# Performance work log

Measured on AMD Instinct MI355X. Metric: run time of the kernel, lower is better.

Reference implementation:

```python
import jax, jax.numpy as jnp
import numpy as np


def setup_inputs() -> dict:
    key = jax.random.key(0)
    k1, k2, k3 = jax.random.split(key, 3)
    N, D_IN, D_OUT = 16384, 512, 128
    inputs = jax.random.normal(k1, (N, D_IN), dtype=jnp.float32)
    adj = jax.random.uniform(k2, (N, N), dtype=jnp.float32)
    # Glorot-uniform init as in weight_variable_glorot
    init_range = np.sqrt(6.0 / (D_IN + D_OUT))
    weights = jax.random.uniform(k3, (D_IN, D_OUT), dtype=jnp.float32,
                                 minval=-init_range, maxval=init_range)
    return {"inputs": inputs, "adj": adj, "weights": weights}


def reference(inputs, adj, weights):
    # x = inputs.to_dense(); x = x @ W; out = adj @ x
    x = jnp.matmul(inputs, weights)      # [N, D_out]
    outputs = jnp.matmul(adj, x)         # [N, D_out]
    return outputs
```

## Files before the change

kernel.cpp:

```cpp
#include <hip/hip_runtime.h>

#define NN 16384
#define DIN 512
#define DOUT 128

typedef __bf16 bf16x8 __attribute__((ext_vector_type(8)));
typedef float floatx4 __attribute__((ext_vector_type(4)));

__device__ __forceinline__ unsigned short f2bf(float f) {
    unsigned u = __builtin_bit_cast(unsigned, f);
    u += 0x7FFFu + ((u >> 16) & 1u);
    return (unsigned short)(u >> 16);
}

__global__ __launch_bounds__(256) void xw_kernel(
        const float* __restrict__ inp, const float* __restrict__ w,
        unsigned short* __restrict__ xT) {
    __shared__ float sIn[32][68];
    __shared__ float sW[64][128];
    const int tid = threadIdx.x;
    const int n0 = blockIdx.x * 32;
    const int tn = tid >> 4;
    const int td = tid & 15;

    float acc[2][8];
#pragma unroll
    for (int i = 0; i < 2; ++i)
#pragma unroll
        for (int j = 0; j < 8; ++j) acc[i][j] = 0.f;

    for (int c0 = 0; c0 < DIN; c0 += 64) {
        __syncthreads();
#pragma unroll
        for (int p = 0; p < 2; ++p) {
            int s = tid + p * 256;
            int row = s >> 4, c4 = (s & 15) << 2;
            *(float4*)&sIn[row][c4] =
                *(const float4*)&inp[(size_t)(n0 + row) * DIN + c0 + c4];
        }
#pragma unroll
        for (int p = 0; p < 8; ++p) {
            int s = tid + p * 256;
            int row = s >> 5, c4 = (s & 31) << 2;
            *(float4*)&sW[row][c4] =
                *(const float4*)&w[(size_t)(c0 + row) * DOUT + c4];
        }
        __syncthreads();
#pragma unroll 8
        for (int cc = 0; cc < 64; ++cc) {
            float a0 = sIn[tn * 2 + 0][cc];
            float a1 = sIn[tn * 2 + 1][cc];
            float4 b0 = *(const float4*)&sW[cc][td * 8];
            float4 b1 = *(const float4*)&sW[cc][td * 8 + 4];
            float bb[8] = {b0.x, b0.y, b0.z, b0.w, b1.x, b1.y, b1.z, b1.w};
#pragma unroll
            for (int j = 0; j < 8; ++j) {
                acc[0][j] += a0 * bb[j];
                acc[1][j] += a1 * bb[j];
            }
        }
    }
#pragma unroll
    for (int i = 0; i < 2; ++i)
#pragma unroll
        for (int j = 0; j < 8; ++j) {
            int d = td * 8 + j;
            xT[(size_t)d * NN + n0 + tn * 2 + i] = f2bf(acc[i][j]);
        }
}

__global__ __launch_bounds__(512, 2) void adj_gemm(
        const float* __restrict__ adj, const unsigned short* __restrict__ xT,
        float* __restrict__ out) {
    __shared__ unsigned short As[64][72];
    __shared__ unsigned short Bs[128][72];
    const int tid  = threadIdx.x;
    const int m0   = blockIdx.x * 64;
    const int w    = tid >> 6;
    const int lane = tid & 63;
    const int rt   = w & 3;
    const int cg   = w >> 2;
    const int lm   = lane & 15;
    const int quad = lane >> 4;

    const int arow = tid >> 4;
    const int ac4  = (tid & 15) << 2;
    const int brow = tid >> 3;
    const int bc8  = (tid & 7) << 3;

    const floatx4 zero = {0.f, 0.f, 0.f, 0.f};
    floatx4 acc[4] = {zero, zero, zero, zero};

    float4 ra[2];
    uint4  rb[2];
#pragma unroll
    for (int p = 0; p < 2; ++p)
        ra[p] = *(const float4*)&adj[(size_t)(m0 + arow + p * 32) * NN + ac4];
#pragma unroll
    for (int p = 0; p < 2; ++p)
        rb[p] = *(const uint4*)&xT[(size_t)(brow + p * 64) * NN + bc8];

    for (int kt = 0; kt < NN / 64; ++kt) {
        __syncthreads();
#pragma unroll
        for (int p = 0; p < 2; ++p) {
            ushort4 h;
            h.x = f2bf(ra[p].x); h.y = f2bf(ra[p].y);
            h.z = f2bf(ra[p].z); h.w = f2bf(ra[p].w);
            *(ushort4*)&As[arow + p * 32][ac4] = h;
        }
#pragma unroll
        for (int p = 0; p < 2; ++p)
            *(uint4*)&Bs[brow + p * 64][bc8] = rb[p];
        __syncthreads();
        if (kt + 1 < NN / 64) {
            const int k0 = (kt + 1) * 64;
#pragma unroll
            for (int p = 0; p < 2; ++p)
                ra[p] = *(const float4*)&adj[(size_t)(m0 + arow + p * 32) * NN + k0 + ac4];
#pragma unroll
            for (int p = 0; p < 2; ++p)
                rb[p] = *(const uint4*)&xT[(size_t)(brow + p * 64) * NN + k0 + bc8];
        }
#pragma unroll
        for (int kk = 0; kk < 2; ++kk) {
            bf16x8 a = *(const bf16x8*)&As[rt * 16 + lm][kk * 32 + quad * 8];
#pragma unroll
            for (int t = 0; t < 4; ++t) {
                bf16x8 b = *(const bf16x8*)&Bs[cg * 64 + t * 16 + lm][kk * 32 + quad * 8];
                acc[t] = __builtin_amdgcn_mfma_f32_16x16x32_bf16(a, b, acc[t], 0, 0, 0);
            }
        }
    }
#pragma unroll
    for (int t = 0; t < 4; ++t)
#pragma unroll
        for (int r = 0; r < 4; ++r)
            out[(size_t)(m0 + rt * 16 + quad * 4 + r) * DOUT + cg * 64 + t * 16 + lm] =
                acc[t][r];
}

extern "C" void kernel_launch(void* const* d_in, const int* in_sizes, int n_in,
                              void* d_out, int out_size, void* d_ws, size_t ws_size,
                              hipStream_t stream) {
    const float* inputs  = (const float*)d_in[0];
    const float* adj     = (const float*)d_in[1];
    const float* weights = (const float*)d_in[2];
    float* out = (float*)d_out;
    unsigned short* xT = (unsigned short*)d_ws;

    xw_kernel<<<NN / 32, 256, 0, stream>>>(inputs, weights, xT);
    adj_gemm<<<NN / 64, 512, 0, stream>>>(adj, xT, out);
}
```

Measured before the change: 1.749 ms.

## Pre-swizzle X into MFMA fragment layout, drop LDS, and split-K the adj GEMM

The xw kernel now writes X in a fragment-ordered bf16 layout, so the adj GEMM can load B operands straight from global into registers without LDS staging or barriers. Each wave handles 16 rows against all 128 output columns, with register double-buffering of adj and X fragments. K is split in two across blockIdx.y into fp32 partial buffers, and a separate reduce kernel sums them. The aim is to remove LDS round-trips and syncs and to raise parallelism. The cost is an extra 16 MB of partial writes and reads, a third launch, and uncoalesced per-row adj loads (32 bytes per lane spread across rows).

```diff
diff --git a/kernel.cpp b/kernel.cpp
--- a/kernel.cpp
+++ b/kernel.cpp
@@ -3,6 +3,9 @@
 #define NN 16384
 #define DIN 512
 #define DOUT 128
+#define SPLITK 2
+#define KHALF (NN / SPLITK)
+#define NK32 (KHALF / 32)
 
 typedef __bf16 bf16x8 __attribute__((ext_vector_type(8)));
 typedef float floatx4 __attribute__((ext_vector_type(4)));
@@ -13,30 +16,36 @@
     return (unsigned short)(u >> 16);
 }
 
+__device__ __forceinline__ unsigned pk2(float lo, float hi) {
+    return (unsigned)f2bf(lo) | ((unsigned)f2bf(hi) << 16);
+}
+
 __global__ __launch_bounds__(256) void xw_kernel(
         const float* __restrict__ inp, const float* __restrict__ w,
-        unsigned short* __restrict__ xT) {
-    __shared__ float sIn[32][68];
+        unsigned short* __restrict__ xTf) {
+    __shared__ float sInT[64][36];
     __shared__ float sW[64][128];
     const int tid = threadIdx.x;
     const int n0 = blockIdx.x * 32;
-    const int tn = tid >> 4;
-    const int td = tid & 15;
+    const int ng = tid >> 6;
+    const int dp = tid & 63;
 
-    float acc[2][8];
+    float acc[8][2];
 #pragma unroll
-    for (int i = 0; i < 2; ++i)
-#pragma unroll
-        for (int j = 0; j < 8; ++j) acc[i][j] = 0.f;
+    for (int i = 0; i < 8; ++i) { acc[i][0] = 0.f; acc[i][1] = 0.f; }
 
     for (int c0 = 0; c0 < DIN; c0 += 64) {
         __syncthreads();
 #pragma unroll
         for (int p = 0; p < 2; ++p) {
             int s = tid + p * 256;
-            int row = s >> 4, c4 = (s & 15) << 2;
-            *(float4*)&sIn[row][c4] =
-                *(const float4*)&inp[(size_t)(n0 + row) * DIN + c0 + c4];
+            int row = s >> 4;
+            int c4 = (s & 15) << 2;
+            float4 v = *(const float4*)&inp[(size_t)(n0 + row) * DIN + c0 + c4];
+            sInT[c4 + 0][row] = v.x;
+            sInT[c4 + 1][row] = v.y;
+            sInT[c4 + 2][row] = v.z;
+            sInT[c4 + 3][row] = v.w;
         }
 #pragma unroll
         for (int p = 0; p < 8; ++p) {
@@ -46,98 +55,103 @@
                 *(const float4*)&w[(size_t)(c0 + row) * DOUT + c4];
         }
         __syncthreads();
-#pragma unroll 8
+#pragma unroll 4
         for (int cc = 0; cc < 64; ++cc) {
-            float a0 = sIn[tn * 2 + 0][cc];
-            float a1 = sIn[tn * 2 + 1][cc];
-            float4 b0 = *(const float4*)&sW[cc][td * 8];
-            float4 b1 = *(const float4*)&sW[cc][td * 8 + 4];
-            float bb[8] = {b0.x, b0.y, b0.z, b0.w, b1.x, b1.y, b1.z, b1.w};
+            float4 a0 = *(const float4*)&sInT[cc][ng * 8];
+            float4 a1 = *(const float4*)&sInT[cc][ng * 8 + 4];
+            float2 b = *(const float2*)&sW[cc][dp * 2];
+            float av[8] = {a0.x, a0.y, a0.z, a0.w, a1.x, a1.y, a1.z, a1.w};
 #pragma unroll
-            for (int j = 0; j < 8; ++j) {
-                acc[0][j] += a0 * bb[j];
-                acc[1][j] += a1 * bb[j];
+            for (int i = 0; i < 8; ++i) {
+                acc[i][0] += av[i] * b.x;
+                acc[i][1] += av[i] * b.y;
             }
         }
     }
 #pragma unroll
-    for (int i = 0; i < 2; ++i)
-#pragma unroll
-        for (int j = 0; j < 8; ++j) {
-            int d = td * 8 + j;
-            xT[(size_t)d * NN + n0 + tn * 2 + i] = f2bf(acc[i][j]);
-        }
+    for (int j = 0; j < 2; ++j) {
+        int d = dp * 2 + j;
+        uint4 u;
+        u.x = pk2(acc[0][j], acc[1][j]);
+        u.y = pk2(acc[2][j], acc[3][j]);
+        u.z = pk2(acc[4][j], acc[5][j]);
+        u.w = pk2(acc[6][j], acc[7][j]);
+        size_t off16 = ((size_t)blockIdx.x * 8 + (d >> 4)) * 64
+                       + (ng * 16 + (d & 15));
+        ((uint4*)xTf)[off16] = u;
+    }
 }
 
-__global__ __launch_bounds__(512, 2) void adj_gemm(
-        const float* __restrict__ adj, const unsigned short* __restrict__ xT,
-        float* __restrict__ out) {
-    __shared__ unsigned short As[64][72];
-    __shared__ unsigned short Bs[128][72];
-    const int tid  = threadIdx.x;
-    const int m0   = blockIdx.x * 64;
-    const int w    = tid >> 6;
+__global__ __launch_bounds__(256, 2) void adj_gemm_f(
+        const float* __restrict__ adj, const unsigned short* __restrict__ xTf,
+        float* __restrict__ part) {
+    const int tid = threadIdx.x;
+    const int w = tid >> 6;
     const int lane = tid & 63;
-    const int rt   = w & 3;
-    const int cg   = w >> 2;
-    const int lm   = lane & 15;
+    const int lm = lane & 15;
     const int quad = lane >> 4;
+    const int m0 = blockIdx.x * 64;
+    const int sk = blockIdx.y;
+    const int row = m0 + w * 16 + lm;
 
-    const int arow = tid >> 4;
-    const int ac4  = (tid & 15) << 2;
-    const int brow = tid >> 3;
-    const int bc8  = (tid & 7) << 3;
+    const float* ap = adj + (size_t)row * NN + (size_t)sk * KHALF + quad * 8;
+    const uint4* bp = (const uint4*)xTf + (size_t)sk * NK32 * 512 + lane;
 
-    const floatx4 zero = {0.f, 0.f, 0.f, 0.f};
-    floatx4 acc[4] = {zero, zero, zero, zero};
+    floatx4 acc[8];
+#pragma unroll
+    for (int t = 0; t < 8; ++t) acc[t] = (floatx4){0.f, 0.f, 0.f, 0.f};
 
-    float4 ra[2];
-    uint4  rb[2];
+    float4 a0A, a1A; uint4 bA[8];
+    float4 a0B, a1B; uint4 bB[8];
+
+#define LOADK(S, kk) do {                                                    \
+        const float* _a = ap + (size_t)(kk) * 32;                            \
+        a0##S = *(const float4*)_a;                                          \
+        a1##S = *(const float4*)(_a + 4);                                    \
+        const uint4* _b = bp + (size_t)(kk) * 512;                           \
+        _Pragma("unroll")                                                    \
+        for (int t = 0; t < 8; ++t) b##S[t] = _b[t * 64];                    \
+    } while (0)
+
+#define COMPUTE(S) do {                                                      \
+        bf16x8 a;                                                            \
+        a[0] = (__bf16)a0##S.x; a[1] = (__bf16)a0##S.y;                      \
+        a[2] = (__bf16)a0##S.z; a[3] = (__bf16)a0##S.w;                      \
+        a[4] = (__bf16)a1##S.x; a[5] = (__bf16)a1##S.y;                      \
+        a[6] = (__bf16)a1##S.z; a[7] = (__bf16)a1##S.w;                      \
+        _Pragma("unroll")                                                    \
+        for (int t = 0; t < 8; ++t)                                          \
+            acc[t] = __builtin_amdgcn_mfma_f32_16x16x32_bf16(                \
+                a, __builtin_bit_cast(bf16x8, b##S[t]), acc[t], 0, 0, 0);    \
+    } while (0)
+
+    LOADK(A, 0);
+    for (int k = 0; k < NK32; k += 2) {
+        LOADK(B, k + 1);
+        COMPUTE(A);
+        if (k + 2 < NK32) LOADK(A, k + 2);
+        COMPUTE(B);
+    }
+#undef LOADK
+#undef COMPUTE
+
+    float* po = part + (size_t)sk * NN * DOUT;
 #pragma unroll
-    for (int p = 0; p < 2; ++p)
-        ra[p] = *(const float4*)&adj[(size_t)(m0 + arow + p * 32) * NN + ac4];
-#pragma unroll
-    for (int p = 0; p < 2; ++p)
-        rb[p] = *(const uint4*)&xT[(size_t)(brow + p * 64) * NN + bc8];
-
-    for (int kt = 0; kt < NN / 64; ++kt) {
-        __syncthreads();
-#pragma unroll
-        for (int p = 0; p < 2; ++p) {
-            ushort4 h;
-            h.x = f2bf(ra[p].x); h.y = f2bf(ra[p].y);
-            h.z = f2bf(ra[p].z); h.w = f2bf(ra[p].w);
-            *(ushort4*)&As[arow + p * 32][ac4] = h;
-        }
-#pragma unroll
-        for (int p = 0; p < 2; ++p)
-            *(uint4*)&Bs[brow + p * 64][bc8] = rb[p];
-        __syncthreads();
-        if (kt + 1 < NN / 64) {
-            const int k0 = (kt + 1) * 64;
-#pragma unroll
-            for (int p = 0; p < 2; ++p)
-                ra[p] = *(const float4*)&adj[(size_t)(m0 + arow + p * 32) * NN + k0 + ac4];
-#pragma unroll
-            for (int p = 0; p < 2; ++p)
-                rb[p] = *(const uint4*)&xT[(size_t)(brow + p * 64) * NN + k0 + bc8];
-        }
-#pragma unroll
-        for (int kk = 0; kk < 2; ++kk) {
-            bf16x8 a = *(const bf16x8*)&As[rt * 16 + lm][kk * 32 + quad * 8];
-#pragma unroll
-            for (int t = 0; t < 4; ++t) {
-                bf16x8 b = *(const bf16x8*)&Bs[cg * 64 + t * 16 + lm][kk * 32 + quad * 8];
-                acc[t] = __builtin_amdgcn_mfma_f32_16x16x32_bf16(a, b, acc[t], 0, 0, 0);
-            }
-        }
-    }
-#pragma unroll
-    for (int t = 0; t < 4; ++t)
+    for (int t = 0; t < 8; ++t)
 #pragma unroll
         for (int r = 0; r < 4; ++r)
-            out[(size_t)(m0 + rt * 16 + quad * 4 + r) * DOUT + cg * 64 + t * 16 + lm] =
+            po[(size_t)(m0 + w * 16 + quad * 4 + r) * DOUT + t * 16 + lm] =
                 acc[t][r];
+}
+
+__global__ __launch_bounds__(256) void reduce_k(
+        const float* __restrict__ part, float* __restrict__ out) {
+    size_t i = (size_t)blockIdx.x * 256 + threadIdx.x;
+    const float4* p0 = (const float4*)part;
+    const float4* p1 = (const float4*)(part + (size_t)NN * DOUT);
+    float4 a = p0[i], b = p1[i];
+    float4 r = {a.x + b.x, a.y + b.y, a.z + b.z, a.w + b.w};
+    ((float4*)out)[i] = r;
 }
 
 extern "C" void kernel_launch(void* const* d_in, const int* in_sizes, int n_in,
@@ -147,8 +161,11 @@
     const float* adj     = (const float*)d_in[1];
     const float* weights = (const float*)d_in[2];
     float* out = (float*)d_out;
-    unsigned short* xT = (unsigned short*)d_ws;
 
-    xw_kernel<<<NN / 32, 256, 0, stream>>>(inputs, weights, xT);
-    adj_gemm<<<NN / 64, 512, 0, stream>>>(adj, xT, out);
+    unsigned short* xTf = (unsigned short*)d_ws;
+    float* part = (float*)((char*)d_ws + (4u << 20));
+
+    xw_kernel<<<NN / 32, 256, 0, stream>>>(inputs, weights, xTf);
+    adj_gemm_f<<<dim3(NN / 64, SPLITK), 256, 0, stream>>>(adj, xTf, part);
+    reduce_k<<<(NN * DOUT / 4) / 256, 256, 0, stream>>>(part, out);
 }
```

Measured after the change: 1.601 ms. 8.5% less time.
